# Kernel tuning notes

Measured on AMD Instinct MI355X. Metric: run time of the kernel, lower is better.

The kernel has to match this reference:

```python
import jax, jax.numpy as jnp
import numpy as np

B, A, D, H, S, C, NB = 8192, 8, 4096, 1024, 32, 32, 8
BS = D // NB          # 512: hidden block size
IBS = (2 * H) // NB   # 256: input block size (gru input = action_embed ++ stoch_embed)
UNIMIX = 0.01


def setup_inputs() -> dict:
    key = jax.random.key(0)
    ks = jax.random.split(key, 16)
    rn = lambda k, shape, s=1.0: jax.random.normal(k, shape, jnp.float32) * s
    return {
        'deterministic': rn(ks[0], (B, D)),
        'stochastic': jax.random.uniform(ks[1], (B, S, C), jnp.float32),
        'prev_action': rn(ks[2], (B, A)),
        'embed': rn(ks[3], (B, H)),
        'is_first': jax.random.bernoulli(ks[4], 0.1, (B,)),
        # encoders (nn.Linear stores weight as [out, in])
        'W_act': rn(ks[5], (H, A), 1.0 / np.sqrt(A)), 'b_act': jnp.zeros((H,)),
        'W_stoch': rn(ks[6], (H, S * C), 1.0 / np.sqrt(S * C)), 'b_stoch': jnp.zeros((H,)),
        # block-diagonal GRU: per-block [3*BS, IBS] and [3*BS, BS]
        'W_ih': rn(ks[7], (NB, 3 * BS, IBS), 1.0 / np.sqrt(IBS)), 'b_ih': jnp.zeros((NB, 3 * BS)),
        'W_hh': rn(ks[8], (NB, 3 * BS, BS), 1.0 / np.sqrt(BS)), 'b_hh': jnp.zeros((NB, 3 * BS)),
        # prior net: D -> H -> S*C
        'W_pr1': rn(ks[9], (H, D), 1.0 / np.sqrt(D)), 'b_pr1': jnp.zeros((H,)),
        'W_pr2': rn(ks[10], (S * C, H), 1.0 / np.sqrt(H)), 'b_pr2': jnp.zeros((S * C,)),
        # posterior net: D+H -> H -> S*C
        'W_po1': rn(ks[11], (H, D + H), 1.0 / np.sqrt(D + H)), 'b_po1': jnp.zeros((H,)),
        'W_po2': rn(ks[12], (S * C, H), 1.0 / np.sqrt(H)), 'b_po2': jnp.zeros((S * C,)),
    }


def _forward(deterministic, stochastic, prev_action, embed, is_first,
             W_act, b_act, W_stoch, b_stoch, W_ih, b_ih, W_hh, b_hh,
             W_pr1, b_pr1, W_pr2, b_pr2, W_po1, b_po1, W_po2, b_po2):
    # reset state where is_first (initial_state is all zeros)
    det = jnp.where(is_first[:, None], 0.0, deterministic)
    stoch = jnp.where(is_first[:, None, None], 0.0, stochastic)
    # action normalization (magnitude detached)
    mag = jnp.maximum(jnp.max(jnp.abs(prev_action), axis=-1, keepdims=True), 1.0)
    act = prev_action / jax.lax.stop_gradient(mag)
    # encoders
    ae = act @ W_act.T + b_act                         # [B, H]
    se = stoch.reshape(stoch.shape[0], -1) @ W_stoch.T + b_stoch  # [B, H]
    x = jnp.concatenate([ae, se], axis=-1)             # [B, 2H]
    # block-diagonal GRU: batched small GEMMs over NB blocks
    xb = x.reshape(-1, NB, IBS)
    hb = det.reshape(-1, NB, BS)
    gates = (jnp.einsum('bki,koi->bko', xb, W_ih) + b_ih
             + jnp.einsum('bkj,koj->bko', hb, W_hh) + b_hh)  # [B, NB, 3*BS]
    gates = gates.reshape(-1, NB, 3, BS)
    reset = jax.nn.sigmoid(gates[:, :, 0])
    update = jax.nn.sigmoid(gates[:, :, 1])
    cand = jnp.tanh(reset * gates[:, :, 2])
    h_new = ((1.0 - update) * hb + update * cand).reshape(-1, D)  # [B, D]
    # prior head
    ph = jax.nn.silu(h_new @ W_pr1.T + b_pr1)
    prior_logits = ph @ W_pr2.T + b_pr2                # [B, S*C]
    pp = jax.nn.softmax(prior_logits.reshape(-1, S, C), axis=-1)
    prior_probs = ((1.0 - UNIMIX) * pp + UNIMIX / C).reshape(-1, S * C)
    # posterior head
    qh = jax.nn.silu(jnp.concatenate([h_new, embed], axis=-1) @ W_po1.T + b_po1)
    post_logits = qh @ W_po2.T + b_po2                 # [B, S*C]
    return jnp.concatenate([h_new, prior_logits, prior_probs, post_logits], axis=-1)


def reference(deterministic, stochastic, prev_action, embed, is_first,
              W_act, b_act, W_stoch, b_stoch, W_ih, b_ih, W_hh, b_hh,
              W_pr1, b_pr1, W_pr2, b_pr2, W_po1, b_po1, W_po2, b_po2):
    return _forward(deterministic, stochastic, prev_action, embed, is_first,
                    W_act, b_act, W_stoch, b_stoch, W_ih, b_ih, W_hh, b_hh,
                    W_pr1, b_pr1, W_pr2, b_pr2, W_po1, b_po1, W_po2, b_po2)
```

## Files before the change

kernel.cpp:

```cpp
#include <hip/hip_runtime.h>

typedef unsigned short u16;
typedef short bf16x8 __attribute__((ext_vector_type(8)));
typedef float f32x4 __attribute__((ext_vector_type(4)));

#define BSZ 8192
#define OUTLD 7168

__device__ __forceinline__ u16 f2bf(float f) {
  union { float f; unsigned u; } v; v.f = f;
  unsigned r = v.u + 0x7FFFu + ((v.u >> 16) & 1u);
  return (u16)(r >> 16);
}
__device__ __forceinline__ float bf2f(u16 h) {
  union { unsigned u; float f; } v; v.u = ((unsigned)h) << 16;
  return v.f;
}
__device__ __forceinline__ float sigmoidf_(float x) { return 1.0f / (1.0f + __expf(-x)); }
__device__ __forceinline__ float tanhf_(float t) { return 2.0f / (1.0f + __expf(-2.0f * t)) - 1.0f; }

__device__ __forceinline__ void gload16(const u16* g, u16* l) {
  __builtin_amdgcn_global_load_lds(
      (const __attribute__((address_space(1))) void*)g,
      (__attribute__((address_space(3))) void*)l, 16, 0, 0);
}

__global__ void k_detect(const unsigned* __restrict__ isf, int* __restrict__ flag) {
  __shared__ unsigned red;
  if (threadIdx.x == 0) red = 0u;
  __syncthreads();
  unsigned v = 0;
  for (int i = threadIdx.x; i < 2048; i += 256) v |= isf[i];
  atomicOr(&red, v);
  __syncthreads();
  if (threadIdx.x == 0)
    *flag = (((red & 0xFFFFFF00u) != 0u) && ((red & 0xFEFEFEFEu) == 0u)) ? 1 : 0;
}

__device__ __forceinline__ bool is_first_row(const void* isf, int fl, int b) {
  return fl ? (((const unsigned char*)isf)[b] != 0) : (((const int*)isf)[b] != 0);
}

struct Cv7 { const float* s[7]; u16* d[7]; long n4[7]; };
__global__ void k_cvtW(Cv7 c, long total4) {
  long stride = (long)gridDim.x * blockDim.x;
  for (long i = blockIdx.x * (long)blockDim.x + threadIdx.x; i < total4; i += stride) {
    long rem = i; int k = 0;
    while (k < 6 && rem >= c.n4[k]) { rem -= c.n4[k]; ++k; }
    float4 v = ((const float4*)c.s[k])[rem];
    ushort4 o; o.x = f2bf(v.x); o.y = f2bf(v.y); o.z = f2bf(v.z); o.w = f2bf(v.w);
    ((ushort4*)c.d[k])[rem] = o;
  }
}

struct Prep3 { const float* s[3]; u16* d[3]; long n4[3]; int c4[3]; int doR[3]; };
__global__ void k_prep(Prep3 p, const void* __restrict__ isf, const int* __restrict__ flag) {
  int fl = *flag;
  long stride = (long)gridDim.x * blockDim.x;
  long gid = blockIdx.x * (long)blockDim.x + threadIdx.x;
#pragma unroll 1
  for (int k = 0; k < 3; ++k) {
    const float4* src = (const float4*)p.s[k];
    ushort4* dst = (ushort4*)p.d[k];
    long n = p.n4[k]; int c4 = p.c4[k], doR = p.doR[k];
    for (long i = gid; i < n; i += stride) {
      float4 v = src[i];
      if (doR && is_first_row(isf, fl, (int)(i / c4))) { v.x = v.y = v.z = v.w = 0.f; }
      ushort4 o; o.x = f2bf(v.x); o.y = f2bf(v.y); o.z = f2bf(v.z); o.w = f2bf(v.w);
      dst[i] = o;
    }
  }
}

__global__ void k_ae(const float* __restrict__ act, const float* __restrict__ Wact,
                     const float* __restrict__ bact, u16* __restrict__ x) {
  long stride = (long)gridDim.x * blockDim.x;
  for (long t = blockIdx.x * (long)blockDim.x + threadIdx.x; t < (long)BSZ * 256; t += stride) {
    int b = (int)(t >> 8), h0 = (int)(t & 255) * 4;
    float4 a0 = ((const float4*)act)[b * 2];
    float4 a1 = ((const float4*)act)[b * 2 + 1];
    float mag = fmaxf(
        fmaxf(fmaxf(fabsf(a0.x), fabsf(a0.y)), fmaxf(fabsf(a0.z), fabsf(a0.w))),
        fmaxf(fmaxf(fabsf(a1.x), fabsf(a1.y)), fmaxf(fabsf(a1.z), fabsf(a1.w))));
    float inv = 1.0f / fmaxf(mag, 1.0f);
    ushort4 o;
    u16* op = (u16*)&o;
#pragma unroll
    for (int j = 0; j < 4; ++j) {
      int h = h0 + j;
      float4 w0 = ((const float4*)Wact)[h * 2];
      float4 w1 = ((const float4*)Wact)[h * 2 + 1];
      float dot = a0.x * w0.x + a0.y * w0.y + a0.z * w0.z + a0.w * w0.w
                + a1.x * w1.x + a1.y * w1.y + a1.z * w1.z + a1.w * w1.w;
      op[j] = f2bf(dot * inv + bact[h]);
    }
    *(ushort4*)&x[(long)b * 2048 + h0] = o;
  }
}

struct GDesc {
  const u16* A1; const u16* A2;
  int lda1, lda2, K1, K2;
  const u16* W1; const u16* W2;
  int ldw1, ldw2;
  const float* bias;
  float* outF; int ldoF;
  u16* outB; int ldoB;
  int actSilu;
};

__global__ __launch_bounds__(256, 3) void gemm128(GDesc d0, GDesc d1) {
  const GDesc d = blockIdx.z ? d1 : d0;
  __shared__ __align__(16) u16 lsA[128 * 64];
  __shared__ __align__(16) u16 lsB[128 * 64];
  const int tid = threadIdx.x;
  const int wave = tid >> 6, lane = tid & 63;
  const int m0 = blockIdx.x * 128, n0 = blockIdx.y * 128;
  const int wr = (wave >> 1) * 64, wc = (wave & 1) * 64;
  const int lrow = lane & 15;
  const int lq = lane >> 4;
  const int lr7 = lrow & 7;
  const int grow = wave * 8 + (lane >> 3);
  const int gcol = ((lane & 7) ^ (lane >> 3)) * 8;
  const int ro0 = ((lq ^ lr7)) * 8;
  const int ro1 = (((4 | lq) ^ lr7)) * 8;

  const f32x4 z4 = {0.f, 0.f, 0.f, 0.f};
  f32x4 acc[4][4];
#pragma unroll
  for (int m = 0; m < 4; ++m)
#pragma unroll
    for (int c = 0; c < 4; ++c) acc[m][c] = z4;

#pragma unroll 1
  for (int phse = 0; phse < 2; ++phse) {
    const u16* A = phse ? d.A2 : d.A1;
    const u16* W = phse ? d.W2 : d.W1;
    const int lda = phse ? d.lda2 : d.lda1;
    const int ldw = phse ? d.ldw2 : d.ldw1;
    const int K = phse ? d.K2 : d.K1;
#pragma unroll 1
    for (int k0 = 0; k0 < K; k0 += 64) {
      __syncthreads();
#pragma unroll
      for (int i = 0; i < 4; ++i) {
        gload16(&A[(long)(m0 + i * 32 + grow) * lda + k0 + gcol], &lsA[i * 2048 + wave * 512]);
        gload16(&W[(long)(n0 + i * 32 + grow) * ldw + k0 + gcol], &lsB[i * 2048 + wave * 512]);
      }
      __syncthreads();
#pragma unroll
      for (int kk = 0; kk < 2; ++kk) {
        const int ro = kk ? ro1 : ro0;
        bf16x8 af[4], wfr[4];
#pragma unroll
        for (int m = 0; m < 4; ++m)
          af[m] = *(const bf16x8*)&lsA[(wr + m * 16 + lrow) * 64 + ro];
#pragma unroll
        for (int c = 0; c < 4; ++c)
          wfr[c] = *(const bf16x8*)&lsB[(wc + c * 16 + lrow) * 64 + ro];
#pragma unroll
        for (int m = 0; m < 4; ++m)
#pragma unroll
          for (int c = 0; c < 4; ++c)
            acc[m][c] = __builtin_amdgcn_mfma_f32_16x16x32_bf16(af[m], wfr[c], acc[m][c], 0, 0, 0);
      }
    }
  }

#pragma unroll
  for (int c = 0; c < 4; ++c) {
    const int col = n0 + wc + c * 16 + lrow;
    const float bv = d.bias ? d.bias[col] : 0.f;
#pragma unroll
    for (int m = 0; m < 4; ++m) {
      const int rowb = m0 + wr + m * 16 + (lane >> 4) * 4;
#pragma unroll
      for (int r = 0; r < 4; ++r) {
        float v = acc[m][c][r] + bv;
        if (d.actSilu) v = v * sigmoidf_(v);
        if (d.outF) d.outF[(long)(rowb + r) * d.ldoF + col] = v;
        if (d.outB) d.outB[(long)(rowb + r) * d.ldoB + col] = f2bf(v);
      }
    }
  }
}

__global__ __launch_bounds__(512, 4) void gru128(
    const u16* __restrict__ xbuf, const u16* __restrict__ hbuf,
    const u16* __restrict__ Wih, const u16* __restrict__ Whh,
    const float* __restrict__ bih, const float* __restrict__ bhh,
    float* __restrict__ outF, u16* __restrict__ hnew)
{
  __shared__ __align__(16) u16 lsA[128 * 64];
  __shared__ __align__(16) u16 lsW[3 * 64 * 64];
  const int tid = threadIdx.x;
  const int wave = tid >> 6, lane = tid & 63;
  const int wm = wave & 3;
  const int ws = wave >> 2;
  const int m0 = blockIdx.x * 128;
  const int blk = blockIdx.y >> 3;
  const int s0 = (blockIdx.y & 7) * 64;
  const int lrow = lane & 15;
  const int lq = lane >> 4;
  const int lr7 = lrow & 7;
  const int gcol = ((lane & 7) ^ (lane >> 3)) * 8;
  const int ro0 = ((lq ^ lr7)) * 8;
  const int ro1 = (((4 | lq) ^ lr7)) * 8;

  const f32x4 z4 = {0.f, 0.f, 0.f, 0.f};
  f32x4 acc[3][2][2];
#pragma unroll
  for (int g = 0; g < 3; ++g)
#pragma unroll
    for (int m = 0; m < 2; ++m)
#pragma unroll
      for (int c = 0; c < 2; ++c) acc[g][m][c] = z4;

#pragma unroll 1
  for (int phse = 0; phse < 2; ++phse) {
    const u16* A = phse ? (hbuf + blk * 512) : (xbuf + blk * 256);
    const u16* W = phse ? (Whh + (long)blk * 1536 * 512) : (Wih + (long)blk * 1536 * 256);
    const int lda = phse ? 4096 : 2048;
    const int ldw = phse ? 512 : 256;
    const int K = phse ? 512 : 256;
#pragma unroll 1
    for (int k0 = 0; k0 < K; k0 += 64) {
      __syncthreads();
#pragma unroll
      for (int r = 0; r < 2; ++r) {
        const int chunk = r * 8 + wave;
        gload16(&A[(long)(m0 + chunk * 8 + (lane >> 3)) * lda + k0 + gcol], &lsA[chunk * 512]);
      }
#pragma unroll
      for (int r = 0; r < 3; ++r) {
        const int chunk = r * 8 + wave;
        const int g = chunk >> 3;
        const int r0 = (chunk & 7) * 8;
        gload16(&W[(long)(g * 512 + s0 + r0 + (lane >> 3)) * ldw + k0 + gcol], &lsW[chunk * 512]);
      }
      __syncthreads();
#pragma unroll
      for (int kk = 0; kk < 2; ++kk) {
        const int ro = kk ? ro1 : ro0;
        bf16x8 af[2], wfr[3][2];
#pragma unroll
        for (int m = 0; m < 2; ++m)
          af[m] = *(const bf16x8*)&lsA[(wm * 32 + m * 16 + lrow) * 64 + ro];
#pragma unroll
        for (int g = 0; g < 3; ++g)
#pragma unroll
          for (int c = 0; c < 2; ++c)
            wfr[g][c] = *(const bf16x8*)&lsW[g * 4096 + (ws * 32 + c * 16 + lrow) * 64 + ro];
#pragma unroll
        for (int g = 0; g < 3; ++g)
#pragma unroll
          for (int m = 0; m < 2; ++m)
#pragma unroll
            for (int c = 0; c < 2; ++c)
              acc[g][m][c] = __builtin_amdgcn_mfma_f32_16x16x32_bf16(af[m], wfr[g][c], acc[g][m][c], 0, 0, 0);
      }
    }
  }

#pragma unroll
  for (int c = 0; c < 2; ++c) {
    const int s = s0 + ws * 32 + c * 16 + lrow;
    const int bb = blk * 1536 + s;
    const float br = bih[bb] + bhh[bb];
    const float bu = bih[bb + 512] + bhh[bb + 512];
    const float bc = bih[bb + 1024] + bhh[bb + 1024];
    const int hcol = blk * 512 + s;
#pragma unroll
    for (int m = 0; m < 2; ++m) {
      const int rowb = m0 + wm * 32 + m * 16 + lq * 4;
#pragma unroll
      for (int r = 0; r < 4; ++r) {
        const int row = rowb + r;
        const float gr = acc[0][m][c][r] + br;
        const float gu = acc[1][m][c][r] + bu;
        const float gc = acc[2][m][c][r] + bc;
        const float rr = sigmoidf_(gr);
        const float uu = sigmoidf_(gu);
        const float cand = tanhf_(rr * gc);
        const float h = bf2f(hbuf[(long)row * 4096 + hcol]);
        const float hn = (1.f - uu) * h + uu * cand;
        outF[(long)row * OUTLD + hcol] = hn;
        hnew[(long)row * 4096 + hcol] = f2bf(hn);
      }
    }
  }
}

__global__ void k_softmax(float* __restrict__ out) {
  int t = blockIdx.x * blockDim.x + threadIdx.x;
  if (t >= BSZ * 32) return;
  int b = t >> 5, g = t & 31;
  const float* src = out + (long)b * OUTLD + 4096 + g * 32;
  float* dst = out + (long)b * OUTLD + 5120 + g * 32;
  float v[32];
#pragma unroll
  for (int i = 0; i < 8; ++i) {
    float4 q = ((const float4*)src)[i];
    v[4 * i] = q.x; v[4 * i + 1] = q.y; v[4 * i + 2] = q.z; v[4 * i + 3] = q.w;
  }
  float m = v[0];
#pragma unroll
  for (int i = 1; i < 32; ++i) m = fmaxf(m, v[i]);
  float ssum = 0.f;
#pragma unroll
  for (int i = 0; i < 32; ++i) { v[i] = __expf(v[i] - m); ssum += v[i]; }
  float inv = 0.99f / ssum;
#pragma unroll
  for (int i = 0; i < 8; ++i) {
    float4 q;
    q.x = v[4 * i] * inv + 3.125e-4f;
    q.y = v[4 * i + 1] * inv + 3.125e-4f;
    q.z = v[4 * i + 2] * inv + 3.125e-4f;
    q.w = v[4 * i + 3] * inv + 3.125e-4f;
    ((float4*)dst)[i] = q;
  }
}

extern "C" void kernel_launch(void* const* d_in, const int* in_sizes, int n_in,
                              void* d_out, int out_size, void* d_ws, size_t ws_size,
                              hipStream_t stream) {
  const float* det   = (const float*)d_in[0];
  const float* stoch = (const float*)d_in[1];
  const float* pact  = (const float*)d_in[2];
  const float* embed = (const float*)d_in[3];
  const void*  isf   = d_in[4];
  const float* Wact  = (const float*)d_in[5];
  const float* bact  = (const float*)d_in[6];
  const float* Wst   = (const float*)d_in[7];
  const float* bst   = (const float*)d_in[8];
  const float* Wih   = (const float*)d_in[9];
  const float* bih   = (const float*)d_in[10];
  const float* Whh   = (const float*)d_in[11];
  const float* bhh   = (const float*)d_in[12];
  const float* Wpr1  = (const float*)d_in[13];
  const float* bpr1  = (const float*)d_in[14];
  const float* Wpr2  = (const float*)d_in[15];
  const float* bpr2  = (const float*)d_in[16];
  const float* Wpo1  = (const float*)d_in[17];
  const float* bpo1  = (const float*)d_in[18];
  const float* Wpo2  = (const float*)d_in[19];
  const float* bpo2  = (const float*)d_in[20];
  float* out = (float*)d_out;

  int* flag = (int*)d_ws;
  u16* wsu  = (u16*)((char*)d_ws + 256);
  u16* bWst  = wsu;
  u16* bWih  = wsu + 1048576UL;
  u16* bWhh  = wsu + 4194304UL;
  u16* bWpr1 = wsu + 10485760UL;
  u16* bWpr2 = wsu + 14680064UL;
  u16* bWpo1 = wsu + 15728640UL;
  u16* bWpo2 = wsu + 20971520UL;
  u16* bufX  = wsu + 22020096UL;
  u16* bufSt = wsu + 38797312UL;
  u16* bufHb = wsu + 47185920UL;
  u16* bufHn = wsu + 80740352UL;
  u16* bufEm = wsu + 114294784UL;

  k_detect<<<dim3(1), dim3(256), 0, stream>>>((const unsigned*)isf, flag);

  Cv7 cw;
  cw.s[0] = Wst;  cw.d[0] = bWst;  cw.n4[0] = 262144L;
  cw.s[1] = Wih;  cw.d[1] = bWih;  cw.n4[1] = 786432L;
  cw.s[2] = Whh;  cw.d[2] = bWhh;  cw.n4[2] = 1572864L;
  cw.s[3] = Wpr1; cw.d[3] = bWpr1; cw.n4[3] = 1048576L;
  cw.s[4] = Wpr2; cw.d[4] = bWpr2; cw.n4[4] = 262144L;
  cw.s[5] = Wpo1; cw.d[5] = bWpo1; cw.n4[5] = 1310720L;
  cw.s[6] = Wpo2; cw.d[6] = bWpo2; cw.n4[6] = 262144L;
  k_cvtW<<<dim3(2048), dim3(256), 0, stream>>>(cw, 5505024L);

  Prep3 pp;
  pp.s[0] = stoch; pp.d[0] = bufSt; pp.n4[0] = 2097152L; pp.c4[0] = 256;  pp.doR[0] = 1;
  pp.s[1] = det;   pp.d[1] = bufHb; pp.n4[1] = 8388608L; pp.c4[1] = 1024; pp.doR[1] = 1;
  pp.s[2] = embed; pp.d[2] = bufEm; pp.n4[2] = 2097152L; pp.c4[2] = 256;  pp.doR[2] = 0;
  k_prep<<<dim3(4096), dim3(256), 0, stream>>>(pp, isf, flag);

  k_ae<<<dim3(2048), dim3(256), 0, stream>>>(pact, Wact, bact, bufX);

  GDesc dSe;
  dSe.A1 = bufSt; dSe.A2 = nullptr; dSe.lda1 = 1024; dSe.lda2 = 0;
  dSe.K1 = 1024; dSe.K2 = 0;
  dSe.W1 = bWst; dSe.W2 = nullptr; dSe.ldw1 = 1024; dSe.ldw2 = 0;
  dSe.bias = bst; dSe.outF = nullptr; dSe.ldoF = 0;
  dSe.outB = bufX + 1024; dSe.ldoB = 2048; dSe.actSilu = 0;
  gemm128<<<dim3(64, 8, 1), dim3(256), 0, stream>>>(dSe, dSe);

  gru128<<<dim3(64, 64), dim3(512), 0, stream>>>(bufX, bufHb, bWih, bWhh, bih, bhh, out, bufHn);

  GDesc dPr1, dPo1;
  dPr1.A1 = bufHn; dPr1.A2 = nullptr; dPr1.lda1 = 4096; dPr1.lda2 = 0;
  dPr1.K1 = 4096; dPr1.K2 = 0;
  dPr1.W1 = bWpr1; dPr1.W2 = nullptr; dPr1.ldw1 = 4096; dPr1.ldw2 = 0;
  dPr1.bias = bpr1; dPr1.outF = nullptr; dPr1.ldoF = 0;
  dPr1.outB = bufSt; dPr1.ldoB = 1024; dPr1.actSilu = 1;
  dPo1.A1 = bufHn; dPo1.A2 = bufEm; dPo1.lda1 = 4096; dPo1.lda2 = 1024;
  dPo1.K1 = 4096; dPo1.K2 = 1024;
  dPo1.W1 = bWpo1; dPo1.W2 = bWpo1 + 4096; dPo1.ldw1 = 5120; dPo1.ldw2 = 5120;
  dPo1.bias = bpo1; dPo1.outF = nullptr; dPo1.ldoF = 0;
  dPo1.outB = bufHb; dPo1.ldoB = 1024; dPo1.actSilu = 1;
  gemm128<<<dim3(64, 8, 2), dim3(256), 0, stream>>>(dPr1, dPo1);

  GDesc dPr2, dPo2;
  dPr2.A1 = bufSt; dPr2.A2 = nullptr; dPr2.lda1 = 1024; dPr2.lda2 = 0;
  dPr2.K1 = 1024; dPr2.K2 = 0;
  dPr2.W1 = bWpr2; dPr2.W2 = nullptr; dPr2.ldw1 = 1024; dPr2.ldw2 = 0;
  dPr2.bias = bpr2; dPr2.outF = out + 4096; dPr2.ldoF = OUTLD;
  dPr2.outB = nullptr; dPr2.ldoB = 0; dPr2.actSilu = 0;
  dPo2.A1 = bufHb; dPo2.A2 = nullptr; dPo2.lda1 = 1024; dPo2.lda2 = 0;
  dPo2.K1 = 1024; dPo2.K2 = 0;
  dPo2.W1 = bWpo2; dPo2.W2 = nullptr; dPo2.ldw1 = 1024; dPo2.ldw2 = 0;
  dPo2.bias = bpo2; dPo2.outF = out + 6144; dPo2.ldoF = OUTLD;
  dPo2.outB = nullptr; dPo2.ldoB = 0; dPo2.actSilu = 0;
  gemm128<<<dim3(64, 8, 2), dim3(256), 0, stream>>>(dPr2, dPo2);

  k_softmax<<<dim3(1024), dim3(256), 0, stream>>>(out);
}
```

Measured before the change: 713.9 us.

## Pre-permute GRU weights gate-interleaved and shrink GRU tile to 128x96

Adds a conversion kernel that reorders the block-diagonal GRU weights so each 32-column slice holds its reset/update/candidate rows contiguously. The GRU kernel then loads one contiguous 96-row weight tile instead of three strided gate slices. It also switches from 512-thread 128x192 tiles to 256-thread 128x96 tiles with a different per-wave split. This gives more blocks and less LDS per block, at the cost of reloading the activation tile twice as often.

```diff
diff --git a/kernel.cpp b/kernel.cpp
--- a/kernel.cpp
+++ b/kernel.cpp
@@ -41,15 +41,37 @@
   return fl ? (((const unsigned char*)isf)[b] != 0) : (((const int*)isf)[b] != 0);
 }
 
-struct Cv7 { const float* s[7]; u16* d[7]; long n4[7]; };
-__global__ void k_cvtW(Cv7 c, long total4) {
+struct Cv5 { const float* s[5]; u16* d[5]; long n4[5]; };
+__global__ void k_cvtW(Cv5 c, long total4) {
   long stride = (long)gridDim.x * blockDim.x;
   for (long i = blockIdx.x * (long)blockDim.x + threadIdx.x; i < total4; i += stride) {
     long rem = i; int k = 0;
-    while (k < 6 && rem >= c.n4[k]) { rem -= c.n4[k]; ++k; }
+    while (k < 4 && rem >= c.n4[k]) { rem -= c.n4[k]; ++k; }
     float4 v = ((const float4*)c.s[k])[rem];
     ushort4 o; o.x = f2bf(v.x); o.y = f2bf(v.y); o.z = f2bf(v.z); o.w = f2bf(v.w);
     ((ushort4*)c.d[k])[rem] = o;
+  }
+}
+
+__global__ void k_cvt_gruW(const float* __restrict__ sIh, u16* __restrict__ dIh,
+                           const float* __restrict__ sHh, u16* __restrict__ dHh) {
+  const long nIh = 393216L, total = 1179648L;
+  long stride = (long)gridDim.x * blockDim.x;
+  for (long i = blockIdx.x * (long)blockDim.x + threadIdx.x; i < total; i += stride) {
+    const float* src; u16* dst; int ldk; long rel;
+    if (i < nIh) { src = sIh; dst = dIh; ldk = 256; rel = i; }
+    else         { src = sHh; dst = dHh; ldk = 512; rel = i - nIh; }
+    int kc = ldk >> 3;
+    int j = (int)(rel % kc); long row = rel / kc;
+    long blk = row / 1536; int rP = (int)(row % 1536);
+    int sHi = rP / 48, rem = rP % 48, g = rem >> 4, sLo = rem & 15;
+    int srow = g * 512 + sHi * 16 + sLo;
+    const float* s = src + (blk * 1536 + srow) * (long)ldk + j * 8;
+    float4 v0 = ((const float4*)s)[0], v1 = ((const float4*)s)[1];
+    ushort4 o0; o0.x = f2bf(v0.x); o0.y = f2bf(v0.y); o0.z = f2bf(v0.z); o0.w = f2bf(v0.w);
+    ushort4 o1; o1.x = f2bf(v1.x); o1.y = f2bf(v1.y); o1.z = f2bf(v1.z); o1.w = f2bf(v1.w);
+    ((ushort4*)(dst + rel * 8))[0] = o0;
+    ((ushort4*)(dst + rel * 8))[1] = o1;
   }
 }
 
@@ -185,41 +207,40 @@
   }
 }
 
-__global__ __launch_bounds__(512, 4) void gru128(
+__global__ __launch_bounds__(256, 4) void gru96(
     const u16* __restrict__ xbuf, const u16* __restrict__ hbuf,
-    const u16* __restrict__ Wih, const u16* __restrict__ Whh,
+    const u16* __restrict__ WihP, const u16* __restrict__ WhhP,
     const float* __restrict__ bih, const float* __restrict__ bhh,
     float* __restrict__ outF, u16* __restrict__ hnew)
 {
   __shared__ __align__(16) u16 lsA[128 * 64];
-  __shared__ __align__(16) u16 lsW[3 * 64 * 64];
+  __shared__ __align__(16) u16 lsW[96 * 64];
   const int tid = threadIdx.x;
   const int wave = tid >> 6, lane = tid & 63;
-  const int wm = wave & 3;
-  const int ws = wave >> 2;
+  const int wm = wave >> 1;
+  const int wn = wave & 1;
   const int m0 = blockIdx.x * 128;
-  const int blk = blockIdx.y >> 3;
-  const int s0 = (blockIdx.y & 7) * 64;
+  const int blk = blockIdx.y >> 4;
+  const int sp = blockIdx.y & 15;
   const int lrow = lane & 15;
   const int lq = lane >> 4;
-  const int lr7 = lrow & 7;
+  const int lr7 = lane & 7;
   const int gcol = ((lane & 7) ^ (lane >> 3)) * 8;
   const int ro0 = ((lq ^ lr7)) * 8;
   const int ro1 = (((4 | lq) ^ lr7)) * 8;
 
   const f32x4 z4 = {0.f, 0.f, 0.f, 0.f};
-  f32x4 acc[3][2][2];
-#pragma unroll
-  for (int g = 0; g < 3; ++g)
-#pragma unroll
-    for (int m = 0; m < 2; ++m)
-#pragma unroll
-      for (int c = 0; c < 2; ++c) acc[g][m][c] = z4;
+  f32x4 acc[4][3];
+#pragma unroll
+  for (int m = 0; m < 4; ++m)
+#pragma unroll
+    for (int g = 0; g < 3; ++g) acc[m][g] = z4;
 
 #pragma unroll 1
   for (int phse = 0; phse < 2; ++phse) {
     const u16* A = phse ? (hbuf + blk * 512) : (xbuf + blk * 256);
-    const u16* W = phse ? (Whh + (long)blk * 1536 * 512) : (Wih + (long)blk * 1536 * 256);
+    const u16* W = phse ? (WhhP + (long)blk * 786432 + sp * 49152)
+                        : (WihP + (long)blk * 393216 + sp * 24576);
     const int lda = phse ? 4096 : 2048;
     const int ldw = phse ? 512 : 256;
     const int K = phse ? 512 : 256;
@@ -227,66 +248,57 @@
     for (int k0 = 0; k0 < K; k0 += 64) {
       __syncthreads();
 #pragma unroll
-      for (int r = 0; r < 2; ++r) {
-        const int chunk = r * 8 + wave;
+      for (int r = 0; r < 4; ++r) {
+        const int chunk = r * 4 + wave;
         gload16(&A[(long)(m0 + chunk * 8 + (lane >> 3)) * lda + k0 + gcol], &lsA[chunk * 512]);
       }
 #pragma unroll
       for (int r = 0; r < 3; ++r) {
-        const int chunk = r * 8 + wave;
-        const int g = chunk >> 3;
-        const int r0 = (chunk & 7) * 8;
-        gload16(&W[(long)(g * 512 + s0 + r0 + (lane >> 3)) * ldw + k0 + gcol], &lsW[chunk * 512]);
+        const int chunk = r * 4 + wave;
+        gload16(&W[(long)(chunk * 8 + (lane >> 3)) * ldw + k0 + gcol], &lsW[chunk * 512]);
       }
       __syncthreads();
 #pragma unroll
       for (int kk = 0; kk < 2; ++kk) {
         const int ro = kk ? ro1 : ro0;
-        bf16x8 af[2], wfr[3][2];
-#pragma unroll
-        for (int m = 0; m < 2; ++m)
-          af[m] = *(const bf16x8*)&lsA[(wm * 32 + m * 16 + lrow) * 64 + ro];
+        bf16x8 af[4], wf[3];
+#pragma unroll
+        for (int m = 0; m < 4; ++m)
+          af[m] = *(const bf16x8*)&lsA[(wm * 64 + m * 16 + lrow) * 64 + ro];
 #pragma unroll
         for (int g = 0; g < 3; ++g)
-#pragma unroll
-          for (int c = 0; c < 2; ++c)
-            wfr[g][c] = *(const bf16x8*)&lsW[g * 4096 + (ws * 32 + c * 16 + lrow) * 64 + ro];
-#pragma unroll
-        for (int g = 0; g < 3; ++g)
-#pragma unroll
-          for (int m = 0; m < 2; ++m)
-#pragma unroll
-            for (int c = 0; c < 2; ++c)
-              acc[g][m][c] = __builtin_amdgcn_mfma_f32_16x16x32_bf16(af[m], wfr[g][c], acc[g][m][c], 0, 0, 0);
-      }
-    }
-  }
-
-#pragma unroll
-  for (int c = 0; c < 2; ++c) {
-    const int s = s0 + ws * 32 + c * 16 + lrow;
-    const int bb = blk * 1536 + s;
-    const float br = bih[bb] + bhh[bb];
-    const float bu = bih[bb + 512] + bhh[bb + 512];
-    const float bc = bih[bb + 1024] + bhh[bb + 1024];
-    const int hcol = blk * 512 + s;
-#pragma unroll
-    for (int m = 0; m < 2; ++m) {
-      const int rowb = m0 + wm * 32 + m * 16 + lq * 4;
-#pragma unroll
-      for (int r = 0; r < 4; ++r) {
-        const int row = rowb + r;
-        const float gr = acc[0][m][c][r] + br;
-        const float gu = acc[1][m][c][r] + bu;
-        const float gc = acc[2][m][c][r] + bc;
-        const float rr = sigmoidf_(gr);
-        const float uu = sigmoidf_(gu);
-        const float cand = tanhf_(rr * gc);
-        const float h = bf2f(hbuf[(long)row * 4096 + hcol]);
-        const float hn = (1.f - uu) * h + uu * cand;
-        outF[(long)row * OUTLD + hcol] = hn;
-        hnew[(long)row * 4096 + hcol] = f2bf(hn);
-      }
+          wf[g] = *(const bf16x8*)&lsW[(wn * 48 + g * 16 + lrow) * 64 + ro];
+#pragma unroll
+        for (int m = 0; m < 4; ++m)
+#pragma unroll
+          for (int g = 0; g < 3; ++g)
+            acc[m][g] = __builtin_amdgcn_mfma_f32_16x16x32_bf16(af[m], wf[g], acc[m][g], 0, 0, 0);
+      }
+    }
+  }
+
+  const int s = sp * 32 + wn * 16 + lrow;
+  const int col = blk * 512 + s;
+  const long bb = (long)blk * 1536 + s;
+  const float br = bih[bb] + bhh[bb];
+  const float bu = bih[bb + 512] + bhh[bb + 512];
+  const float bc = bih[bb + 1024] + bhh[bb + 1024];
+#pragma unroll
+  for (int m = 0; m < 4; ++m) {
+    const int rowb = m0 + wm * 64 + m * 16 + lq * 4;
+#pragma unroll
+    for (int r = 0; r < 4; ++r) {
+      const int row = rowb + r;
+      const float gr = acc[m][0][r] + br;
+      const float gu = acc[m][1][r] + bu;
+      const float gc = acc[m][2][r] + bc;
+      const float rr = sigmoidf_(gr);
+      const float uu = sigmoidf_(gu);
+      const float cand = tanhf_(rr * gc);
+      const float h = bf2f(hbuf[(long)row * 4096 + col]);
+      const float hn = (1.f - uu) * h + uu * cand;
+      outF[(long)row * OUTLD + col] = hn;
+      hnew[(long)row * 4096 + col] = f2bf(hn);
     }
   }
 }
@@ -350,8 +362,8 @@
   int* flag = (int*)d_ws;
   u16* wsu  = (u16*)((char*)d_ws + 256);
   u16* bWst  = wsu;
-  u16* bWih  = wsu + 1048576UL;
-  u16* bWhh  = wsu + 4194304UL;
+  u16* bWihP = wsu + 1048576UL;
+  u16* bWhhP = wsu + 4194304UL;
   u16* bWpr1 = wsu + 10485760UL;
   u16* bWpr2 = wsu + 14680064UL;
   u16* bWpo1 = wsu + 15728640UL;
@@ -364,15 +376,15 @@
 
   k_detect<<<dim3(1), dim3(256), 0, stream>>>((const unsigned*)isf, flag);
 
-  Cv7 cw;
+  Cv5 cw;
   cw.s[0] = Wst;  cw.d[0] = bWst;  cw.n4[0] = 262144L;
-  cw.s[1] = Wih;  cw.d[1] = bWih;  cw.n4[1] = 786432L;
-  cw.s[2] = Whh;  cw.d[2] = bWhh;  cw.n4[2] = 1572864L;
-  cw.s[3] = Wpr1; cw.d[3] = bWpr1; cw.n4[3] = 1048576L;
-  cw.s[4] = Wpr2; cw.d[4] = bWpr2; cw.n4[4] = 262144L;
-  cw.s[5] = Wpo1; cw.d[5] = bWpo1; cw.n4[5] = 1310720L;
-  cw.s[6] = Wpo2; cw.d[6] = bWpo2; cw.n4[6] = 262144L;
-  k_cvtW<<<dim3(2048), dim3(256), 0, stream>>>(cw, 5505024L);
+  cw.s[1] = Wpr1; cw.d[1] = bWpr1; cw.n4[1] = 1048576L;
+  cw.s[2] = Wpr2; cw.d[2] = bWpr2; cw.n4[2] = 262144L;
+  cw.s[3] = Wpo1; cw.d[3] = bWpo1; cw.n4[3] = 1310720L;
+  cw.s[4] = Wpo2; cw.d[4] = bWpo2; cw.n4[4] = 262144L;
+  k_cvtW<<<dim3(2048), dim3(256), 0, stream>>>(cw, 3145728L);
+
+  k_cvt_gruW<<<dim3(2048), dim3(256), 0, stream>>>(Wih, bWihP, Whh, bWhhP);
 
   Prep3 pp;
   pp.s[0] = stoch; pp.d[0] = bufSt; pp.n4[0] = 2097152L; pp.c4[0] = 256;  pp.doR[0] = 1;
@@ -390,7 +402,8 @@
   dSe.outB = bufX + 1024; dSe.ldoB = 2048; dSe.actSilu = 0;
   gemm128<<<dim3(64, 8, 1), dim3(256), 0, stream>>>(dSe, dSe);
 
-  gru128<<<dim3(64, 64), dim3(512), 0, stream>>>(bufX, bufHb, bWih, bWhh, bih, bhh, out, bufHn);
+  gru96<<<dim3(64, 128), dim3(256), 0, stream>>>(bufX, bufHb, bWihP, bWhhP,
+                                                 bih, bhh, out, bufHn);
 
   GDesc dPr1, dPo1;
   dPr1.A1 = bufHn; dPr1.A2 = nullptr; dPr1.lda1 = 4096; dPr1.lda2 = 0;
```

New measurement: 670.2 us. 1.07x faster.
